# Kernel optimization log

Measured on AMD Instinct MI355X. Metric: run time of the kernel, lower is better.

The kernel has to match this reference:

```python
import jax, jax.numpy as jnp
import numpy as np

N_ACT = 6          # n_activated_experts
ROUTE_SCALE = 1.0  # route_scale

def setup_inputs() -> dict:
    key = jax.random.key(0)
    k1, k2 = jax.random.split(key)
    T, D, E = 32768, 2048, 64
    x = jax.random.normal(k1, (T, D), dtype=jnp.float32)
    W = jax.random.normal(k2, (E, D), dtype=jnp.float32) * (1.0 / np.sqrt(D))
    return {"x": x, "W": W}

def reference(x, W):
    # router linear: [T, D] @ [D, E] -> [T, E]
    logits = jnp.einsum('td,ed->te', x, W)
    # softmax in fp32 (matches scores.softmax(dim=-1, dtype=torch.float32))
    probs = jax.nn.softmax(logits.astype(jnp.float32), axis=-1)
    # top-k indices from softmax probabilities
    _, indices = jax.lax.top_k(probs, N_ACT)            # [T, k]
    # gather ORIGINAL (pre-softmax) scores at selected experts, then scale
    weights = jnp.take_along_axis(logits, indices, axis=-1) * ROUTE_SCALE
    return indices, weights
```

## Files before the change

kernel.cpp:

```cpp
#include <hip/hip_runtime.h>

typedef float f32x4 __attribute__((ext_vector_type(4)));
typedef short bf16x8 __attribute__((ext_vector_type(8)));
typedef unsigned int u32;
typedef unsigned short u16;

constexpr int T_ = 32768;
constexpr int D_ = 2048;
constexpr int E_ = 64;
constexpr int KSEL = 6;
constexpr float ROUTE_SCALE_ = 1.0f;

constexpr int ROWS = 64;
constexpr int DK = 32;
constexpr int NCHH = 1024 / DK;
constexpr int WBUF = 12288;
constexpr int HSTRIDE = 2 * WBUF;
constexpr int SLSTR = 66;

__device__ __forceinline__ u16 f2bf(float f) {
  u32 u = __float_as_uint(f);
  return (u16)((u + 0x7fffu + ((u >> 16) & 1u)) >> 16);
}
__device__ __forceinline__ float bf2f(u16 h) { return __uint_as_float(((u32)h) << 16); }

__global__ void wsplit_kernel(const float* __restrict__ W, char* __restrict__ ws) {
  int g = blockIdx.x * 256 + threadIdx.x;
  if (g >= 64 * 256) return;
  int lane = g & 63, nfq = (g >> 6) & 3, c2 = g >> 8;
  int e = nfq * 16 + (lane & 15);
  int k0 = c2 * 32 + ((lane >> 4) << 3);
  const float* src = W + (size_t)e * D_ + k0;
  f32x4 a0 = *(const f32x4*)src;
  f32x4 a1 = *(const f32x4*)(src + 4);
  float f[8] = {a0.x, a0.y, a0.z, a0.w, a1.x, a1.y, a1.z, a1.w};
  bf16x8 h, m, l;
#pragma unroll
  for (int j = 0; j < 8; ++j) {
    u16 hb = f2bf(f[j]); float r1 = f[j] - bf2f(hb);
    u16 mb = f2bf(r1);   float r2 = r1 - bf2f(mb);
    u16 lb = f2bf(r2);
    h[j] = (short)hb; m[j] = (short)mb; l[j] = (short)lb;
  }
  char* dst = ws + (size_t)c2 * WBUF + (size_t)(nfq * 3) * 1024 + lane * 16;
  *(bf16x8*)(dst)        = h;
  *(bf16x8*)(dst + 1024) = m;
  *(bf16x8*)(dst + 2048) = l;
}

__device__ __forceinline__ void gload16(const void* g, void* l) {
  __builtin_amdgcn_global_load_lds(
      (const __attribute__((address_space(1))) void*)g,
      (__attribute__((address_space(3))) void*)l, 16, 0, 0);
}

__launch_bounds__(512, 4)
__global__ void gate_kernel(const float* __restrict__ x, const char* __restrict__ ws,
                            float* __restrict__ out) {
  __shared__ __align__(16) char sm[2 * HSTRIDE];

  const int tid = threadIdx.x;
  const int lane = tid & 63;
  const int wv = tid >> 6;
  const int half = wv >> 2;
  const int wl = wv & 3;
  const int r0 = blockIdx.x * ROWS;

  const float* xp = x + (size_t)(r0 + wl * 16 + (lane & 15)) * D_
                      + half * 1024 + ((lane >> 4) << 3);

  f32x4 xA[2], xB[2];

#define XLOAD(BANK, C)                                            \
  { const float* p_ = xp + (size_t)(C) * DK;                      \
    BANK[0] = *(const f32x4*)(p_); BANK[1] = *(const f32x4*)(p_ + 4); }

  auto wgload = [&](int c2) {
    const char* src = ws + (size_t)(half * NCHH + c2) * WBUF
                         + (size_t)(wl * 64 + lane) * 16;
    char* dstb = sm + half * HSTRIDE + (c2 & 1) * WBUF + (size_t)(wl * 64) * 16;
#pragma unroll
    for (int it = 0; it < 3; ++it)
      gload16(src + it * 4096, dstb + it * 4096);
  };

  f32x4 acc[4] = {};

#define STEP(BANK, C)                                                          \
  {                                                                            \
    bf16x8 ah, am, al;                                                         \
    {                                                                          \
      f32x4 a0 = BANK[0], a1 = BANK[1];                                        \
      float f[8] = {a0.x, a0.y, a0.z, a0.w, a1.x, a1.y, a1.z, a1.w};           \
      _Pragma("unroll")                                                        \
      for (int j = 0; j < 8; ++j) {                                            \
        float v = f[j];                                                        \
        u32 uh = __float_as_uint(v) & 0xffff0000u;                             \
        float r1 = v - __uint_as_float(uh);                                    \
        u32 um = __float_as_uint(r1) & 0xffff0000u;                            \
        float r2 = r1 - __uint_as_float(um);                                   \
        u32 ul = __float_as_uint(r2);                                          \
        ah[j] = (short)(uh >> 16);                                             \
        am[j] = (short)(um >> 16);                                             \
        al[j] = (short)(ul >> 16);                                             \
      }                                                                        \
    }                                                                          \
    const char* wb = sm + half * HSTRIDE + ((C) & 1) * WBUF + lane * 16;       \
    _Pragma("unroll")                                                          \
    for (int n = 0; n < 4; ++n) {                                              \
      const char* fb = wb + (size_t)(n * 3) * 1024;                            \
      bf16x8 bh = *(const bf16x8*)(fb);                                        \
      bf16x8 bm = *(const bf16x8*)(fb + 1024);                                 \
      bf16x8 bl = *(const bf16x8*)(fb + 2048);                                 \
      f32x4 c_ = acc[n];                                                       \
      c_ = __builtin_amdgcn_mfma_f32_16x16x32_bf16(al, bh, c_, 0, 0, 0);       \
      c_ = __builtin_amdgcn_mfma_f32_16x16x32_bf16(am, bm, c_, 0, 0, 0);       \
      c_ = __builtin_amdgcn_mfma_f32_16x16x32_bf16(ah, bl, c_, 0, 0, 0);       \
      c_ = __builtin_amdgcn_mfma_f32_16x16x32_bf16(am, bh, c_, 0, 0, 0);       \
      c_ = __builtin_amdgcn_mfma_f32_16x16x32_bf16(ah, bm, c_, 0, 0, 0);       \
      c_ = __builtin_amdgcn_mfma_f32_16x16x32_bf16(ah, bh, c_, 0, 0, 0);       \
      acc[n] = c_;                                                             \
    }                                                                          \
  }

  XLOAD(xA, 0)
  XLOAD(xB, 1)
  wgload(0);

  for (int cc = 0; cc < NCHH; cc += 2) {
    __syncthreads();
    if (cc + 1 < NCHH) wgload(cc + 1);
    STEP(xA, cc)
    if (cc + 2 < NCHH) XLOAD(xA, cc + 2)
    __syncthreads();
    if (cc + 2 < NCHH) wgload(cc + 2);
    STEP(xB, cc + 1)
    if (cc + 3 < NCHH) XLOAD(xB, cc + 3)
  }

  __syncthreads();
  float* SL = (float*)sm;
#pragma unroll
  for (int n = 0; n < 4; ++n)
#pragma unroll
    for (int j = 0; j < 4; ++j) {
      int r = wl * 16 + ((lane >> 4) << 2) + j;
      int e = n * 16 + (lane & 15);
      SL[half * (E_ * SLSTR) + e * SLSTR + r] = acc[n][j];
    }
  __syncthreads();

  if (wv == 0) {
    float tv[KSEL], ti[KSEL];
#pragma unroll
    for (int kk = 0; kk < KSEL; ++kk) { tv[kk] = -3.4e38f; ti[kk] = 0.f; }
    for (int e = 0; e < E_; ++e) {
      float v = SL[e * SLSTR + lane] + SL[E_ * SLSTR + e * SLSTR + lane];
      float vi = (float)e;
#pragma unroll
      for (int kk = 0; kk < KSEL; ++kk) {
        bool c = v > tv[kk];
        float nv = c ? v : tv[kk];  float dv = c ? tv[kk] : v;
        float ni = c ? vi : ti[kk]; float di = c ? ti[kk] : vi;
        tv[kk] = nv; v = dv; ti[kk] = ni; vi = di;
      }
    }
    const int rg = r0 + lane;
    float* outI = out;
    float* outW = out + (size_t)T_ * KSEL;
#pragma unroll
    for (int kk = 0; kk < KSEL; ++kk) {
      outI[(size_t)rg * KSEL + kk] = ti[kk];
      outW[(size_t)rg * KSEL + kk] = tv[kk] * ROUTE_SCALE_;
    }
  }
#undef XLOAD
#undef STEP
}

extern "C" void kernel_launch(void* const* d_in, const int* in_sizes, int n_in,
                              void* d_out, int out_size, void* d_ws, size_t ws_size,
                              hipStream_t stream) {
  const float* x = (const float*)d_in[0];
  const float* W = (const float*)d_in[1];
  char* ws = (char*)d_ws;
  float* out = (float*)d_out;
  wsplit_kernel<<<dim3(64), dim3(256), 0, stream>>>(W, ws);
  gate_kernel<<<dim3(T_ / ROWS), dim3(512), 0, stream>>>(x, ws, out);
}
```

Before: 72.59 us.

## Triple-buffer W chunks in LDS with explicit vmcnt waits and raw barriers

Replaces the double-buffered W staging loop with a three-slot LDS ring, a four-deep x register rotation, and hand-placed s_waitcnt vmcnt plus s_barrier instead of __syncthreads. The aim is to keep two chunks of global loads in flight while the MFMA work runs, so the full vmcnt drain at each barrier no longer stalls the loop. LDS use per block rises from 48KB to 72KB, which may limit how many blocks fit per CU. Correctness depends on the hand-counted vmcnt values matching the loads actually issued.

```diff
diff --git a/kernel.cpp b/kernel.cpp
--- a/kernel.cpp
+++ b/kernel.cpp
@@ -15,7 +15,7 @@
 constexpr int DK = 32;
 constexpr int NCHH = 1024 / DK;
 constexpr int WBUF = 12288;
-constexpr int HSTRIDE = 2 * WBUF;
+constexpr int HSTRIDE = 3 * WBUF;
 constexpr int SLSTR = 66;
 
 __device__ __forceinline__ u16 f2bf(float f) {
@@ -54,6 +54,10 @@
       (__attribute__((address_space(3))) void*)l, 16, 0, 0);
 }
 
+#define PIN asm volatile("" ::: "memory")
+#define WAITV(N) asm volatile("s_waitcnt vmcnt(" #N ")" ::: "memory")
+#define BAR __builtin_amdgcn_s_barrier()
+
 __launch_bounds__(512, 4)
 __global__ void gate_kernel(const float* __restrict__ x, const char* __restrict__ ws,
                             float* __restrict__ out) {
@@ -69,16 +73,16 @@
   const float* xp = x + (size_t)(r0 + wl * 16 + (lane & 15)) * D_
                       + half * 1024 + ((lane >> 4) << 3);
 
-  f32x4 xA[2], xB[2];
+  f32x4 x0[2], x1[2], x2[2], x3[2];
 
 #define XLOAD(BANK, C)                                            \
   { const float* p_ = xp + (size_t)(C) * DK;                      \
     BANK[0] = *(const f32x4*)(p_); BANK[1] = *(const f32x4*)(p_ + 4); }
 
-  auto wgload = [&](int c2) {
+  auto wgload = [&](int c2, char* dbuf) {
     const char* src = ws + (size_t)(half * NCHH + c2) * WBUF
                          + (size_t)(wl * 64 + lane) * 16;
-    char* dstb = sm + half * HSTRIDE + (c2 & 1) * WBUF + (size_t)(wl * 64) * 16;
+    char* dstb = dbuf + (size_t)(wl * 64) * 16;
 #pragma unroll
     for (int it = 0; it < 3; ++it)
       gload16(src + it * 4096, dstb + it * 4096);
@@ -86,7 +90,7 @@
 
   f32x4 acc[4] = {};
 
-#define STEP(BANK, C)                                                          \
+#define STEP(BANK, RBUF)                                                       \
   {                                                                            \
     bf16x8 ah, am, al;                                                         \
     {                                                                          \
@@ -105,7 +109,7 @@
         al[j] = (short)(ul >> 16);                                             \
       }                                                                        \
     }                                                                          \
-    const char* wb = sm + half * HSTRIDE + ((C) & 1) * WBUF + lane * 16;       \
+    const char* wb = (RBUF) + lane * 16;                                       \
     _Pragma("unroll")                                                          \
     for (int n = 0; n < 4; ++n) {                                              \
       const char* fb = wb + (size_t)(n * 3) * 1024;                            \
@@ -123,20 +127,28 @@
     }                                                                          \
   }
 
-  XLOAD(xA, 0)
-  XLOAD(xB, 1)
-  wgload(0);
-
-  for (int cc = 0; cc < NCHH; cc += 2) {
-    __syncthreads();
-    if (cc + 1 < NCHH) wgload(cc + 1);
-    STEP(xA, cc)
-    if (cc + 2 < NCHH) XLOAD(xA, cc + 2)
-    __syncthreads();
-    if (cc + 2 < NCHH) wgload(cc + 2);
-    STEP(xB, cc + 1)
-    if (cc + 3 < NCHH) XLOAD(xB, cc + 3)
-  }
+  char* base = sm + half * HSTRIDE;
+  char* r0b = base;
+  char* r1b = base + WBUF;
+  char* r2b = base + 2 * WBUF;
+
+  wgload(0, r0b); PIN;
+  XLOAD(x0, 0) XLOAD(x1, 1) wgload(1, r1b); PIN;
+  WAITV(7); BAR;
+
+  for (int g = 0; g < 7; ++g) {
+    const int cc = g * 4;
+    wgload(cc + 2, r2b); PIN; XLOAD(x2, cc + 2) STEP(x0, r0b) WAITV(7); BAR;
+    wgload(cc + 3, r0b); PIN; XLOAD(x3, cc + 3) STEP(x1, r1b) WAITV(7); BAR;
+    wgload(cc + 4, r1b); PIN; XLOAD(x0, cc + 4) STEP(x2, r2b) WAITV(7); BAR;
+    wgload(cc + 5, r2b); PIN; XLOAD(x1, cc + 5) STEP(x3, r0b) WAITV(7); BAR;
+    char* t = r0b; r0b = r1b; r1b = r2b; r2b = t;
+  }
+
+  wgload(30, r2b); PIN; XLOAD(x2, 30) STEP(x0, r0b) WAITV(7); BAR;
+  wgload(31, r0b); PIN; XLOAD(x3, 31) STEP(x1, r1b) WAITV(7); BAR;
+  STEP(x2, r2b) WAITV(2); BAR;
+  STEP(x3, r0b)
 
   __syncthreads();
   float* SL = (float*)sm;
```

New measurement: 75.05 us. +3.4%, slower.

## Split gate GEMM into per-half partial blocks plus separate reduce-topk kernel

Applied to the files above, without the earlier changes.

Splits the fused gate kernel into 256-thread blocks that each compute a 64-row tile over one half of D and write partial logits to workspace. A new reduce_topk kernel sums the two halves and does the top-6 selection with all threads busy, instead of a single wave per block. It also raises MFMA wave priority with s_setprio. The intent is higher occupancy, smaller blocks and less serial top-k tail per block. The cost is an extra launch and 16MB of partial-logit traffic to global memory. If the workspace is too small, the old fused kernel is used instead.

```diff
diff --git a/kernel.cpp b/kernel.cpp
--- a/kernel.cpp
+++ b/kernel.cpp
@@ -17,6 +17,10 @@
 constexpr int WBUF = 12288;
 constexpr int HSTRIDE = 2 * WBUF;
 constexpr int SLSTR = 66;
+
+constexpr size_t WSPLIT_BYTES = 64 * (size_t)WBUF;
+constexpr size_t P_HALF = (size_t)E_ * T_;
+constexpr size_t WS_NEEDED = WSPLIT_BYTES + 2 * P_HALF * 4;
 
 __device__ __forceinline__ u16 f2bf(float f) {
   u32 u = __float_as_uint(f);
@@ -54,39 +58,11 @@
       (__attribute__((address_space(3))) void*)l, 16, 0, 0);
 }
 
-__launch_bounds__(512, 4)
-__global__ void gate_kernel(const float* __restrict__ x, const char* __restrict__ ws,
-                            float* __restrict__ out) {
-  __shared__ __align__(16) char sm[2 * HSTRIDE];
-
-  const int tid = threadIdx.x;
-  const int lane = tid & 63;
-  const int wv = tid >> 6;
-  const int half = wv >> 2;
-  const int wl = wv & 3;
-  const int r0 = blockIdx.x * ROWS;
-
-  const float* xp = x + (size_t)(r0 + wl * 16 + (lane & 15)) * D_
-                      + half * 1024 + ((lane >> 4) << 3);
-
-  f32x4 xA[2], xB[2];
-
 #define XLOAD(BANK, C)                                            \
   { const float* p_ = xp + (size_t)(C) * DK;                      \
     BANK[0] = *(const f32x4*)(p_); BANK[1] = *(const f32x4*)(p_ + 4); }
 
-  auto wgload = [&](int c2) {
-    const char* src = ws + (size_t)(half * NCHH + c2) * WBUF
-                         + (size_t)(wl * 64 + lane) * 16;
-    char* dstb = sm + half * HSTRIDE + (c2 & 1) * WBUF + (size_t)(wl * 64) * 16;
-#pragma unroll
-    for (int it = 0; it < 3; ++it)
-      gload16(src + it * 4096, dstb + it * 4096);
-  };
-
-  f32x4 acc[4] = {};
-
-#define STEP(BANK, C)                                                          \
+#define STEP(BANK, C, WBASE)                                                   \
   {                                                                            \
     bf16x8 ah, am, al;                                                         \
     {                                                                          \
@@ -105,7 +81,8 @@
         al[j] = (short)(ul >> 16);                                             \
       }                                                                        \
     }                                                                          \
-    const char* wb = sm + half * HSTRIDE + ((C) & 1) * WBUF + lane * 16;       \
+    const char* wb = (WBASE) + ((C) & 1) * WBUF + lane * 16;                   \
+    __builtin_amdgcn_s_setprio(1);                                             \
     _Pragma("unroll")                                                          \
     for (int n = 0; n < 4; ++n) {                                              \
       const char* fb = wb + (size_t)(n * 3) * 1024;                            \
@@ -121,7 +98,35 @@
       c_ = __builtin_amdgcn_mfma_f32_16x16x32_bf16(ah, bh, c_, 0, 0, 0);       \
       acc[n] = c_;                                                             \
     }                                                                          \
-  }
+    __builtin_amdgcn_s_setprio(0);                                             \
+  }
+
+__launch_bounds__(256, 4)
+__global__ void gate_partial(const float* __restrict__ x, const char* __restrict__ ws,
+                             float* __restrict__ P) {
+  __shared__ __align__(16) char sm[2 * WBUF];
+
+  const int tid = threadIdx.x;
+  const int lane = tid & 63;
+  const int wl = tid >> 6;
+  const int half = blockIdx.x & 1;
+  const int r0 = (blockIdx.x >> 1) * ROWS;
+
+  const float* xp = x + (size_t)(r0 + wl * 16 + (lane & 15)) * D_
+                      + half * 1024 + ((lane >> 4) << 3);
+
+  f32x4 xA[2], xB[2];
+
+  auto wgload = [&](int c2) {
+    const char* src = ws + (size_t)(half * NCHH + c2) * WBUF
+                         + (size_t)(wl * 64 + lane) * 16;
+    char* dstb = sm + (c2 & 1) * WBUF + (size_t)(wl * 64) * 16;
+#pragma unroll
+    for (int it = 0; it < 3; ++it)
+      gload16(src + it * 4096, dstb + it * 4096);
+  };
+
+  f32x4 acc[4] = {};
 
   XLOAD(xA, 0)
   XLOAD(xB, 1)
@@ -130,11 +135,100 @@
   for (int cc = 0; cc < NCHH; cc += 2) {
     __syncthreads();
     if (cc + 1 < NCHH) wgload(cc + 1);
-    STEP(xA, cc)
+    STEP(xA, cc, sm)
     if (cc + 2 < NCHH) XLOAD(xA, cc + 2)
     __syncthreads();
     if (cc + 2 < NCHH) wgload(cc + 2);
-    STEP(xB, cc + 1)
+    STEP(xB, cc + 1, sm)
+    if (cc + 3 < NCHH) XLOAD(xB, cc + 3)
+  }
+
+  __syncthreads();
+  float* SL = (float*)sm;
+#pragma unroll
+  for (int n = 0; n < 4; ++n)
+#pragma unroll
+    for (int j = 0; j < 4; ++j) {
+      int r = wl * 16 + ((lane >> 4) << 2) + j;
+      int e = n * 16 + (lane & 15);
+      SL[e * SLSTR + r] = acc[n][j];
+    }
+  __syncthreads();
+  float* Pg = P + (size_t)half * P_HALF + r0 + lane;
+#pragma unroll
+  for (int ee = 0; ee < 16; ++ee) {
+    int e = wl * 16 + ee;
+    Pg[(size_t)e * T_] = SL[e * SLSTR + lane];
+  }
+}
+
+__launch_bounds__(128)
+__global__ void reduce_topk(const float* __restrict__ P, float* __restrict__ out) {
+  const int r = blockIdx.x * 128 + threadIdx.x;
+  float tv[KSEL], ti[KSEL];
+#pragma unroll
+  for (int kk = 0; kk < KSEL; ++kk) { tv[kk] = -3.4e38f; ti[kk] = 0.f; }
+  for (int e = 0; e < E_; ++e) {
+    float v = P[(size_t)e * T_ + r] + P[P_HALF + (size_t)e * T_ + r];
+    float vi = (float)e;
+#pragma unroll
+    for (int kk = 0; kk < KSEL; ++kk) {
+      bool c = v > tv[kk];
+      float nv = c ? v : tv[kk];  float dv = c ? tv[kk] : v;
+      float ni = c ? vi : ti[kk]; float di = c ? ti[kk] : vi;
+      tv[kk] = nv; v = dv; ti[kk] = ni; vi = di;
+    }
+  }
+  float* outI = out;
+  float* outW = out + (size_t)T_ * KSEL;
+#pragma unroll
+  for (int kk = 0; kk < KSEL; ++kk) {
+    outI[(size_t)r * KSEL + kk] = ti[kk];
+    outW[(size_t)r * KSEL + kk] = tv[kk] * ROUTE_SCALE_;
+  }
+}
+
+__launch_bounds__(512, 4)
+__global__ void gate_kernel(const float* __restrict__ x, const char* __restrict__ ws,
+                            float* __restrict__ out) {
+  __shared__ __align__(16) char sm[2 * HSTRIDE];
+
+  const int tid = threadIdx.x;
+  const int lane = tid & 63;
+  const int wv = tid >> 6;
+  const int half = wv >> 2;
+  const int wl = wv & 3;
+  const int r0 = blockIdx.x * ROWS;
+
+  const float* xp = x + (size_t)(r0 + wl * 16 + (lane & 15)) * D_
+                      + half * 1024 + ((lane >> 4) << 3);
+
+  f32x4 xA[2], xB[2];
+
+  auto wgload = [&](int c2) {
+    const char* src = ws + (size_t)(half * NCHH + c2) * WBUF
+                         + (size_t)(wl * 64 + lane) * 16;
+    char* dstb = sm + half * HSTRIDE + (c2 & 1) * WBUF + (size_t)(wl * 64) * 16;
+#pragma unroll
+    for (int it = 0; it < 3; ++it)
+      gload16(src + it * 4096, dstb + it * 4096);
+  };
+
+  f32x4 acc[4] = {};
+  char* wbase = sm + half * HSTRIDE;
+
+  XLOAD(xA, 0)
+  XLOAD(xB, 1)
+  wgload(0);
+
+  for (int cc = 0; cc < NCHH; cc += 2) {
+    __syncthreads();
+    if (cc + 1 < NCHH) wgload(cc + 1);
+    STEP(xA, cc, wbase)
+    if (cc + 2 < NCHH) XLOAD(xA, cc + 2)
+    __syncthreads();
+    if (cc + 2 < NCHH) wgload(cc + 2);
+    STEP(xB, cc + 1, wbase)
     if (cc + 3 < NCHH) XLOAD(xB, cc + 3)
   }
 
@@ -174,8 +268,6 @@
       outW[(size_t)rg * KSEL + kk] = tv[kk] * ROUTE_SCALE_;
     }
   }
-#undef XLOAD
-#undef STEP
 }
 
 extern "C" void kernel_launch(void* const* d_in, const int* in_sizes, int n_in,
@@ -186,5 +278,11 @@
   char* ws = (char*)d_ws;
   float* out = (float*)d_out;
   wsplit_kernel<<<dim3(64), dim3(256), 0, stream>>>(W, ws);
-  gate_kernel<<<dim3(T_ / ROWS), dim3(512), 0, stream>>>(x, ws, out);
-}
+  if (ws_size >= WS_NEEDED) {
+    float* P = (float*)(ws + WSPLIT_BYTES);
+    gate_partial<<<dim3(T_ / ROWS * 2), dim3(256), 0, stream>>>(x, ws, P);
+    reduce_topk<<<dim3(T_ / 128), dim3(128), 0, stream>>>(P, out);
+  } else {
+    gate_kernel<<<dim3(T_ / ROWS), dim3(512), 0, stream>>>(x, ws, out);
+  }
+}
```

New measurement: 88.85 us. 22.4% more time.
